# Optimization experiments

Hardware: AMD Instinct MI355X
Metric: run time of the kernel (lower is better)

Reference implementation:

```python
import jax, jax.numpy as jnp
import numpy as np

IN_CH, HID_CH = 32, 64
DILS = (1, 2, 4)


def _conv(x, w, b, dil, pad):
    # x: [B,C,H,W], w: [O,I,kh,kw]
    y = jax.lax.conv_general_dilated(
        x, w, window_strides=(1, 1), padding=[(pad, pad), (pad, pad)],
        rhs_dilation=(dil, dil), dimension_numbers=("NCHW", "OIHW", "NCHW"))
    return y + b[None, :, None, None]


def setup_inputs() -> dict:
    key = jax.random.key(0)
    ks = jax.random.split(key, 9)
    x_seq = jax.random.normal(ks[0], (4, 16, IN_CH, 64, 64), dtype=jnp.float32)
    params = {}
    ch = IN_CH
    for li, _ in enumerate(DILS):
        fan_in = (ch + HID_CH) * 9
        scale = 1.0 / np.sqrt(fan_in)
        params[f"gw{li}"] = jax.random.normal(ks[1 + 2 * li], (4 * HID_CH, ch + HID_CH, 3, 3), jnp.float32) * scale
        params[f"gb{li}"] = jnp.zeros((4 * HID_CH,), jnp.float32)
        ch = HID_CH
    # layer 0 residual 1x1 projection (in_ch != hid_ch)
    params["rw0"] = jax.random.normal(ks[7], (HID_CH, IN_CH, 1, 1), jnp.float32) * (1.0 / np.sqrt(IN_CH))
    params["rb0"] = jnp.zeros((HID_CH,), jnp.float32)
    return {"x_seq": x_seq, **params}


def _run_layer(seq, gw, gb, dil, res_fn):
    # seq: [B,T,C,H,W]
    B, T, C, H, W = seq.shape
    h0 = jnp.zeros((B, HID_CH, H, W), seq.dtype)
    c0 = jnp.zeros_like(h0)

    def step(carry, xt):
        h, c = carry
        g = _conv(jnp.concatenate([xt, h], axis=1), gw, gb, dil, dil)
        i, f, gg, o = jnp.split(g, 4, axis=1)
        c_new = jax.nn.sigmoid(f) * c + jax.nn.sigmoid(i) * jnp.tanh(gg)
        h_new = jax.nn.sigmoid(o) * jnp.tanh(c_new)
        h_out = h_new + res_fn(xt)  # residual added BEFORE next-step carry (matches torch)
        return (h_out, c_new), h_out

    xs = jnp.moveaxis(seq, 1, 0)  # [T,B,C,H,W]
    _, ys = jax.lax.scan(step, (h0, c0), xs)
    return jnp.moveaxis(ys, 0, 1)  # [B,T,hid,H,W]


def reference(x_seq, gw0, gb0, gw1, gb1, gw2, gb2, rw0, rb0):
    res0 = lambda xt: _conv(xt, rw0, rb0, 1, 0)
    ident = lambda xt: xt
    out = _run_layer(x_seq, gw0, gb0, DILS[0], res0)
    out = _run_layer(out, gw1, gb1, DILS[1], ident)
    out = _run_layer(out, gw2, gb2, DILS[2], ident)
    return out
```

## Files before the change

kernel.cpp:

```cpp
#include <hip/hip_runtime.h>
#include <hip/hip_bf16.h>

typedef __bf16 bf16;
typedef __bf16 bf16x8 __attribute__((ext_vector_type(8)));
typedef float f32x4 __attribute__((ext_vector_type(4)));
typedef unsigned short u16;
typedef unsigned short u16x8 __attribute__((ext_vector_type(8)));

#define TT 16
#define BB 4
#define HH 64
#define WW 64
#define HID 64

__device__ __forceinline__ float sigm_f(float x) { return 1.f / (1.f + __expf(-x)); }
__device__ __forceinline__ float tanh_f(float x) { return 1.f - 2.f / (__expf(2.f * x) + 1.f); }

__global__ void xpose_kernel(const float* __restrict__ x, bf16* __restrict__ xb) {
  int idx = blockIdx.x * blockDim.x + threadIdx.x;
  const int total = TT * BB * HH * WW * 32;
  if (idx >= total) return;
  int c = idx & 31;
  int xx = (idx >> 5) & 63;
  int y = (idx >> 11) & 63;
  int b = (idx >> 17) & 3;
  int t = idx >> 19;
  float v = x[((((b * TT + t) * 32 + c) * HH + y) * WW + xx)];
  xb[idx] = (bf16)v;
}

template <int CIN>
__global__ void wprep_kernel(const float* __restrict__ gw, bf16* __restrict__ bmat,
                             const float* __restrict__ rw, bf16* __restrict__ rwb) {
  const int K = CIN * 9;
  int idx = blockIdx.x * blockDim.x + threadIdx.x;
  int total = 256 * K;
  if (idx < total) {
    int n = idx / K;
    int kk = idx - n * K;
    int q = n >> 6, j = n & 63, g = j >> 4, hcl = j & 15;
    int o = g * 64 + q * 16 + hcl;
    int tap = kk / CIN, c = kk - tap * CIN;
    int ky = tap / 3, kx = tap - ky * 3;
    float v = gw[((o * CIN + c) * 3 + ky) * 3 + kx];
    int kt = kk >> 5, kin = kk & 31;
    bmat[(kt * 256 + n) * 32 + kin] = (bf16)v;
  } else if (rw != nullptr) {
    int r = idx - total;
    if (r < 64 * 32) rwb[r] = (bf16)rw[r];
  }
}

template <int L>
__global__ __launch_bounds__(512, 2) void step_kernel(
    const bf16* __restrict__ xsrc, bf16* __restrict__ hbuf,
    const bf16* __restrict__ bmat, const float* __restrict__ gb,
    float* __restrict__ cbuf, const bf16* __restrict__ rwb,
    const float* __restrict__ rb, float* __restrict__ dout, int t) {
  constexpr int Cx = (L == 0) ? 32 : 64;
  constexpr int C = Cx + 64;
  constexpr int DIL = (L == 0) ? 1 : (L == 1 ? 2 : 4);
  constexpr int Wp = WW + 2 * DIL;
  constexpr int KT = (9 * C) / 32;
  constexpr int CT = C / 32;
  constexpr int HS = (L == 2) ? 2 : 16;

  __shared__ __align__(16) char alds[CT * 3 * Wp * 64];

  int bid = blockIdx.x;
  int b = bid >> 6, y = bid & 63;
  int tid = threadIdx.x;
  int lane = tid & 63, wave = tid >> 6;
  int l15 = lane & 15, kgrp = lane >> 4;
  int pxg = wave >> 2, q = wave & 3;

  const char* bmat_c = (const char*)bmat;
  const int voffB = q * 4096 + l15 * 64 + kgrp * 16;

  bf16x8 bfr[4][4];
  auto loadB = [&](int slot, int kt) {
    #pragma unroll
    for (int g = 0; g < 4; ++g)
      bfr[slot][g] = *(const bf16x8*)(bmat_c + (size_t)kt * 16384 + voffB + g * 1024);
  };
  loadB(0, 0);
  loadB(1, 1);

  {
    const int chunks = 3 * Wp * (C / 8);
    for (int i = tid; i < chunks; i += 512) {
      int col = i % Wp;
      int rem = i / Wp;
      int row3 = rem % 3;
      int cg = rem / 3;
      int c = cg * 8;
      int j = cg >> 2, sub = cg & 3;
      int xs = col - DIL;
      int ys = y + (row3 - 1) * DIL;
      u16x8 v = {0, 0, 0, 0, 0, 0, 0, 0};
      if ((unsigned)xs < 64u && (unsigned)ys < 64u) {
        if (c < Cx) {
          v = *(const u16x8*)(xsrc + (size_t)(((t * BB + b) * HH + ys) * WW + xs) * Cx + c);
        } else if (t > 0) {
          int slot = (t - 1) & (HS - 1);
          v = *(const u16x8*)(hbuf + (size_t)(((slot * BB + b) * HH + ys) * WW + xs) * 64 + (c - Cx));
        }
      }
      int off = ((j * 3 + row3) * Wp + col) * 64 + sub * 16;
      off ^= (col & 7) << 4;
      *(u16x8*)(alds + off) = v;
    }
  }
  __syncthreads();

  int abase[2][3];
  #pragma unroll
  for (int m = 0; m < 2; ++m)
    #pragma unroll
    for (int kx = 0; kx < 3; ++kx) {
      int col = pxg * 32 + m * 16 + l15 + kx * DIL;
      abase[m][kx] = (col * 64 + kgrp * 16) ^ ((col & 7) << 4);
    }

  f32x4 acc[2][4];
  #pragma unroll
  for (int m = 0; m < 2; ++m)
    #pragma unroll
    for (int g = 0; g < 4; ++g) acc[m][g] = f32x4{0.f, 0.f, 0.f, 0.f};

  #pragma unroll
  for (int kt = 0; kt < KT; ++kt) {
    if (kt + 2 < KT) loadB((kt + 2) & 3, kt + 2);
    int tap = kt / CT;
    int j = kt - tap * CT;
    int ky = tap / 3, kx = tap - ky * 3;
    int imm = ((j * 3 + ky) * Wp) * 64;
    bf16x8 a0 = *(const bf16x8*)(alds + abase[0][kx] + imm);
    bf16x8 a1 = *(const bf16x8*)(alds + abase[1][kx] + imm);
    #pragma unroll
    for (int g = 0; g < 4; ++g) {
      acc[0][g] = __builtin_amdgcn_mfma_f32_16x16x32_bf16(a0, bfr[kt & 3][g], acc[0][g], 0, 0, 0);
      acc[1][g] = __builtin_amdgcn_mfma_f32_16x16x32_bf16(a1, bfr[kt & 3][g], acc[1][g], 0, 0, 0);
    }
  }

  int hc = q * 16 + l15;
  float bi = gb[hc], bfg = gb[64 + hc], bgg = gb[128 + hc], bog = gb[192 + hc];

  float rwv[32];
  float rbv = 0.f;
  if constexpr (L == 0) {
    rbv = rb[hc];
    const u16x8* rp = (const u16x8*)(rwb + hc * 32);
    #pragma unroll
    for (int p = 0; p < 4; ++p) {
      bf16x8 wb = *(const bf16x8*)(rp + p);
      #pragma unroll
      for (int e = 0; e < 8; ++e) rwv[p * 8 + e] = (float)wb[e];
    }
  }

  #pragma unroll
  for (int m = 0; m < 2; ++m) {
    f32x4 vi = acc[m][0], vf = acc[m][1], vg = acc[m][2], vo = acc[m][3];
    f32x4 hov;
    #pragma unroll
    for (int r = 0; r < 4; ++r) {
      int px = pxg * 32 + m * 16 + kgrp * 4 + r;
      float giv = sigm_f(vi[r] + bi);
      float gfv = sigm_f(vf[r] + bfg);
      float ggv = tanh_f(vg[r] + bgg);
      float gov = sigm_f(vo[r] + bog);
      int cidx = ((b * HH + y) * WW + px) * 64 + hc;
      float cold = (t > 0) ? cbuf[cidx] : 0.f;
      float cn = gfv * cold + giv * ggv;
      cbuf[cidx] = cn;
      float hn = gov * tanh_f(cn);

      float res;
      int colc = px + DIL;
      int swz = (colc & 7) << 4;
      if constexpr (L == 0) {
        float s = rbv;
        #pragma unroll
        for (int kc = 0; kc < 4; ++kc) {
          int off = ((1 * Wp + colc) * 64 + kc * 16) ^ swz;
          bf16x8 xv = *(const bf16x8*)(alds + off);
          #pragma unroll
          for (int e = 0; e < 8; ++e) s += rwv[kc * 8 + e] * (float)xv[e];
        }
        res = s;
      } else {
        int jx = hc >> 5;
        int off = (((jx * 3 + 1) * Wp + colc) * 64 + (hc & 31) * 2) ^ swz;
        res = (float)*(const bf16*)(alds + off);
      }
      float ho = hn + res;
      hov[r] = ho;
      int hslot = t & (HS - 1);
      hbuf[(size_t)(((hslot * BB + b) * HH + y) * WW + px) * 64 + hc] = (bf16)ho;
    }
    if constexpr (L == 2) {
      int px0 = pxg * 32 + m * 16 + kgrp * 4;
      *(f32x4*)(dout + (size_t)(((b * TT + t) * HID + hc) * HH + y) * WW + px0) = hov;
    }
  }
}

extern "C" void kernel_launch(void* const* d_in, const int* in_sizes, int n_in,
                              void* d_out, int out_size, void* d_ws, size_t ws_size,
                              hipStream_t stream) {
  const float* x_seq = (const float*)d_in[0];
  const float* gw0 = (const float*)d_in[1];
  const float* gb0 = (const float*)d_in[2];
  const float* gw1 = (const float*)d_in[3];
  const float* gb1 = (const float*)d_in[4];
  const float* gw2 = (const float*)d_in[5];
  const float* gb2 = (const float*)d_in[6];
  const float* rw0 = (const float*)d_in[7];
  const float* rb0 = (const float*)d_in[8];
  float* dout = (float*)d_out;

  char* ws = (char*)d_ws;
  size_t off = 0;
  auto carve = [&](size_t bytes) {
    char* p = ws + off;
    off += (bytes + 255) & ~(size_t)255;
    return p;
  };
  bf16* xb0 = (bf16*)carve((size_t)TT * BB * HH * WW * 32 * 2);
  bf16* seqA = (bf16*)carve((size_t)TT * BB * HH * WW * 64 * 2);
  bf16* seqB = (bf16*)carve((size_t)TT * BB * HH * WW * 64 * 2);
  bf16* hC = (bf16*)carve((size_t)2 * BB * HH * WW * 64 * 2);
  float* cbuf = (float*)carve((size_t)BB * HH * WW * 64 * 4);
  bf16* bm0 = (bf16*)carve((size_t)27 * 256 * 32 * 2);
  bf16* bm1 = (bf16*)carve((size_t)36 * 256 * 32 * 2);
  bf16* bm2 = (bf16*)carve((size_t)36 * 256 * 32 * 2);
  bf16* rwb = (bf16*)carve((size_t)64 * 32 * 2);

  {
    int total = TT * BB * HH * WW * 32;
    xpose_kernel<<<(total + 255) / 256, 256, 0, stream>>>(x_seq, xb0);
  }
  {
    int total = 256 * 96 * 9 + 64 * 32;
    wprep_kernel<96><<<(total + 255) / 256, 256, 0, stream>>>(gw0, bm0, rw0, rwb);
  }
  {
    int total = 256 * 128 * 9;
    wprep_kernel<128><<<(total + 255) / 256, 256, 0, stream>>>(gw1, bm1, nullptr, nullptr);
    wprep_kernel<128><<<(total + 255) / 256, 256, 0, stream>>>(gw2, bm2, nullptr, nullptr);
  }

  for (int t = 0; t < TT; ++t)
    step_kernel<0><<<BB * HH, 512, 0, stream>>>(xb0, seqA, bm0, gb0, cbuf, rwb, rb0, nullptr, t);
  for (int t = 0; t < TT; ++t)
    step_kernel<1><<<BB * HH, 512, 0, stream>>>(seqA, seqB, bm1, gb1, cbuf, nullptr, nullptr, nullptr, t);
  for (int t = 0; t < TT; ++t)
    step_kernel<2><<<BB * HH, 512, 0, stream>>>(seqB, hC, bm2, gb2, cbuf, nullptr, nullptr, dout, t);
}
```

Measured before the change: 1.246 ms.

## Wavefront-schedule the three LSTM layers diagonally in one fused launch per step

Replaces 48 sequential per-layer launches with 18 launches, each running layer L at timestep d-L at the same time, so up to 768 blocks fill the GPU instead of 256. Each layer gets its own cell-state buffer, and the cell state moves to a channel-major layout so it can be read and written as f32x4 vectors. The B-fragment ring shrinks from 4 to 3 slots to cut registers, and launch bounds rise to 4 blocks per SM. The fused kernel always reserves the largest shared-memory footprint and carries all three layer paths, which may hurt occupancy or register allocation.

Measured after the change: 1.292 ms. +3.7%, slower.

```diff
diff --git a/kernel.cpp b/kernel.cpp
--- a/kernel.cpp
+++ b/kernel.cpp
@@ -52,11 +52,12 @@
 }
 
 template <int L>
-__global__ __launch_bounds__(512, 2) void step_kernel(
+__device__ __forceinline__ void step_body(
+    char* __restrict__ alds,
     const bf16* __restrict__ xsrc, bf16* __restrict__ hbuf,
     const bf16* __restrict__ bmat, const float* __restrict__ gb,
     float* __restrict__ cbuf, const bf16* __restrict__ rwb,
-    const float* __restrict__ rb, float* __restrict__ dout, int t) {
+    const float* __restrict__ rb, float* __restrict__ dout, int t, int bid) {
   constexpr int Cx = (L == 0) ? 32 : 64;
   constexpr int C = Cx + 64;
   constexpr int DIL = (L == 0) ? 1 : (L == 1 ? 2 : 4);
@@ -65,9 +66,6 @@
   constexpr int CT = C / 32;
   constexpr int HS = (L == 2) ? 2 : 16;
 
-  __shared__ __align__(16) char alds[CT * 3 * Wp * 64];
-
-  int bid = blockIdx.x;
   int b = bid >> 6, y = bid & 63;
   int tid = threadIdx.x;
   int lane = tid & 63, wave = tid >> 6;
@@ -77,7 +75,7 @@
   const char* bmat_c = (const char*)bmat;
   const int voffB = q * 4096 + l15 * 64 + kgrp * 16;
 
-  bf16x8 bfr[4][4];
+  bf16x8 bfr[3][4];
   auto loadB = [&](int slot, int kt) {
     #pragma unroll
     for (int g = 0; g < 4; ++g)
@@ -130,7 +128,7 @@
 
   #pragma unroll
   for (int kt = 0; kt < KT; ++kt) {
-    if (kt + 2 < KT) loadB((kt + 2) & 3, kt + 2);
+    if (kt + 2 < KT) loadB((kt + 2) % 3, kt + 2);
     int tap = kt / CT;
     int j = kt - tap * CT;
     int ky = tap / 3, kx = tap - ky * 3;
@@ -139,8 +137,8 @@
     bf16x8 a1 = *(const bf16x8*)(alds + abase[1][kx] + imm);
     #pragma unroll
     for (int g = 0; g < 4; ++g) {
-      acc[0][g] = __builtin_amdgcn_mfma_f32_16x16x32_bf16(a0, bfr[kt & 3][g], acc[0][g], 0, 0, 0);
-      acc[1][g] = __builtin_amdgcn_mfma_f32_16x16x32_bf16(a1, bfr[kt & 3][g], acc[1][g], 0, 0, 0);
+      acc[0][g] = __builtin_amdgcn_mfma_f32_16x16x32_bf16(a0, bfr[kt % 3][g], acc[0][g], 0, 0, 0);
+      acc[1][g] = __builtin_amdgcn_mfma_f32_16x16x32_bf16(a1, bfr[kt % 3][g], acc[1][g], 0, 0, 0);
     }
   }
 
@@ -163,18 +161,20 @@
   #pragma unroll
   for (int m = 0; m < 2; ++m) {
     f32x4 vi = acc[m][0], vf = acc[m][1], vg = acc[m][2], vo = acc[m][3];
-    f32x4 hov;
+    int px0 = pxg * 32 + m * 16 + kgrp * 4;
+    int cidx = ((b * HH + y) * 64 + hc) * 64 + px0;
+    f32x4 cold4 = f32x4{0.f, 0.f, 0.f, 0.f};
+    if (t > 0) cold4 = *(const f32x4*)(cbuf + cidx);
+    f32x4 cn4, hov;
     #pragma unroll
     for (int r = 0; r < 4; ++r) {
-      int px = pxg * 32 + m * 16 + kgrp * 4 + r;
+      int px = px0 + r;
       float giv = sigm_f(vi[r] + bi);
       float gfv = sigm_f(vf[r] + bfg);
       float ggv = tanh_f(vg[r] + bgg);
       float gov = sigm_f(vo[r] + bog);
-      int cidx = ((b * HH + y) * WW + px) * 64 + hc;
-      float cold = (t > 0) ? cbuf[cidx] : 0.f;
-      float cn = gfv * cold + giv * ggv;
-      cbuf[cidx] = cn;
+      float cn = gfv * cold4[r] + giv * ggv;
+      cn4[r] = cn;
       float hn = gov * tanh_f(cn);
 
       float res;
@@ -200,11 +200,32 @@
       int hslot = t & (HS - 1);
       hbuf[(size_t)(((hslot * BB + b) * HH + y) * WW + px) * 64 + hc] = (bf16)ho;
     }
+    *(f32x4*)(cbuf + cidx) = cn4;
     if constexpr (L == 2) {
-      int px0 = pxg * 32 + m * 16 + kgrp * 4;
       *(f32x4*)(dout + (size_t)(((b * TT + t) * HID + hc) * HH + y) * WW + px0) = hov;
     }
   }
+}
+
+__global__ __launch_bounds__(512, 4) void diag_kernel(
+    const bf16* __restrict__ xb0, bf16* __restrict__ seqA, bf16* __restrict__ seqB,
+    bf16* __restrict__ hC,
+    const bf16* __restrict__ bm0, const bf16* __restrict__ bm1, const bf16* __restrict__ bm2,
+    const float* __restrict__ gb0, const float* __restrict__ gb1, const float* __restrict__ gb2,
+    float* __restrict__ cb0, float* __restrict__ cb1, float* __restrict__ cb2,
+    const bf16* __restrict__ rwb, const float* __restrict__ rb0, float* __restrict__ dout,
+    int l0, int t0, int l1, int t1, int l2, int t2) {
+  __shared__ __align__(16) char alds[55296];
+  int seg = blockIdx.x >> 8;
+  int bid = blockIdx.x & 255;
+  int lay = (seg == 0) ? l0 : ((seg == 1) ? l1 : l2);
+  int t = (seg == 0) ? t0 : ((seg == 1) ? t1 : t2);
+  if (lay == 0)
+    step_body<0>(alds, xb0, seqA, bm0, gb0, cb0, rwb, rb0, nullptr, t, bid);
+  else if (lay == 1)
+    step_body<1>(alds, seqA, seqB, bm1, gb1, cb1, nullptr, nullptr, nullptr, t, bid);
+  else
+    step_body<2>(alds, seqB, hC, bm2, gb2, cb2, nullptr, nullptr, dout, t, bid);
 }
 
 extern "C" void kernel_launch(void* const* d_in, const int* in_sizes, int n_in,
@@ -232,7 +253,9 @@
   bf16* seqA = (bf16*)carve((size_t)TT * BB * HH * WW * 64 * 2);
   bf16* seqB = (bf16*)carve((size_t)TT * BB * HH * WW * 64 * 2);
   bf16* hC = (bf16*)carve((size_t)2 * BB * HH * WW * 64 * 2);
-  float* cbuf = (float*)carve((size_t)BB * HH * WW * 64 * 4);
+  float* cb0 = (float*)carve((size_t)BB * HH * WW * 64 * 4);
+  float* cb1 = (float*)carve((size_t)BB * HH * WW * 64 * 4);
+  float* cb2 = (float*)carve((size_t)BB * HH * WW * 64 * 4);
   bf16* bm0 = (bf16*)carve((size_t)27 * 256 * 32 * 2);
   bf16* bm1 = (bf16*)carve((size_t)36 * 256 * 32 * 2);
   bf16* bm2 = (bf16*)carve((size_t)36 * 256 * 32 * 2);
@@ -252,10 +275,17 @@
     wprep_kernel<128><<<(total + 255) / 256, 256, 0, stream>>>(gw2, bm2, nullptr, nullptr);
   }
 
-  for (int t = 0; t < TT; ++t)
-    step_kernel<0><<<BB * HH, 512, 0, stream>>>(xb0, seqA, bm0, gb0, cbuf, rwb, rb0, nullptr, t);
-  for (int t = 0; t < TT; ++t)
-    step_kernel<1><<<BB * HH, 512, 0, stream>>>(seqA, seqB, bm1, gb1, cbuf, nullptr, nullptr, nullptr, t);
-  for (int t = 0; t < TT; ++t)
-    step_kernel<2><<<BB * HH, 512, 0, stream>>>(seqB, hC, bm2, gb2, cbuf, nullptr, nullptr, dout, t);
-}
+  for (int d = 0; d < TT + 2; ++d) {
+    int lays[3], ts[3], na = 0;
+    for (int L = 0; L < 3; ++L) {
+      int tt = d - L;
+      if (tt >= 0 && tt < TT) { lays[na] = L; ts[na] = tt; ++na; }
+    }
+    int l0 = lays[0], t0 = ts[0];
+    int l1 = (na > 1) ? lays[1] : -1, t1 = (na > 1) ? ts[1] : 0;
+    int l2 = (na > 2) ? lays[2] : -1, t2 = (na > 2) ? ts[2] : 0;
+    diag_kernel<<<na * 256, 512, 0, stream>>>(xb0, seqA, seqB, hC, bm0, bm1, bm2,
+                                              gb0, gb1, gb2, cb0, cb1, cb2,
+                                              rwb, rb0, dout, l0, t0, l1, t1, l2, t2);
+  }
+}
```
